# Performance work log

Hardware: AMD Instinct MI355X
Metric: run time of the kernel (lower is better)

The kernel has to match this reference:

```python
import jax, jax.numpy as jnp
import numpy as np

N_NODES = 100000
N_EDGES = 6400000
D_FEAT = 128
HIDDEN = 16


def _gcn_conv(x, row, col, W, b, n):
    # PyG GCNConv: add self-loops, symmetric norm, message from row -> aggregated at col
    h = x @ W  # [N, out]
    loop = jnp.arange(n, dtype=row.dtype)
    r = jnp.concatenate([row, loop])
    c = jnp.concatenate([col, loop])
    ones = jnp.ones(r.shape[0], dtype=x.dtype)
    deg = jax.ops.segment_sum(ones, c, num_segments=n)  # in-degree incl. self-loop
    dinv = jnp.where(deg > 0, jax.lax.rsqrt(deg), 0.0)
    norm = dinv[r] * dinv[c]  # [E+N]
    msg = h[r] * norm[:, None]  # [E+N, out]
    out = jax.ops.segment_sum(msg, c, num_segments=n)
    return out + b


def setup_inputs() -> dict:
    key = jax.random.key(0)
    ks = jax.random.split(key, 8)
    x = jax.random.normal(ks[0], (N_NODES, D_FEAT), dtype=jnp.float32)
    edge_attr = jax.random.normal(ks[1], (N_EDGES, 1), dtype=jnp.float32)
    edge_row = jnp.sort(jax.random.randint(ks[2], (N_EDGES,), 0, N_NODES, dtype=jnp.int32)).astype(jnp.int64)
    edge_col = jax.random.randint(ks[3], (N_EDGES,), 0, N_NODES, dtype=jnp.int32).astype(jnp.int64)
    W1 = jax.random.normal(ks[4], (D_FEAT + 1, HIDDEN), dtype=jnp.float32) * (1.0 / np.sqrt(D_FEAT + 1))
    b1 = jnp.zeros((HIDDEN,), dtype=jnp.float32)
    W2 = jax.random.normal(ks[5], (HIDDEN, 1), dtype=jnp.float32) * (1.0 / np.sqrt(HIDDEN))
    b2 = jnp.zeros((1,), dtype=jnp.float32)
    return {"x": x, "edge_attr": edge_attr, "edge_row": edge_row, "edge_col": edge_col,
            "W1": W1, "b1": b1, "W2": W2, "b2": b2}


def reference(x, edge_attr, edge_row, edge_col, W1, b1, W2, b2):
    n = x.shape[0]
    # the original Python loop == segment-sum of edge_attr by source node (rows are sorted)
    x_edge = jax.ops.segment_sum(edge_attr, edge_row, num_segments=n)  # [N, 1]
    h = jnp.concatenate([x, x_edge], axis=1)  # [N, D+1]
    h = _gcn_conv(h, edge_row, edge_col, W1, b1, n)
    h = jax.nn.relu(h)
    # dropout is identity in eval mode
    out = _gcn_conv(h, edge_row, edge_col, W2, b2, n)  # [N, 1]
    return out
```

## Files before the change

### kernel.cpp

```cpp
#include <hip/hip_runtime.h>


#define D_FEAT 128
#define HIDDEN 16
#define TILE 8192
#define CAP 17408u

__device__ inline float bf2f(unsigned short u) {
    union { unsigned x; float f; } t; t.x = ((unsigned)u) << 16; return t.f;
}

__global__ __launch_bounds__(256) void k_init(float* xe, unsigned* gcur, int n, int nb) {
    int t = blockIdx.x * 256 + threadIdx.x;
    if (t < n) xe[t] = 0.f;
    if (t < nb) gcur[t * 16] = (unsigned)t * CAP;
}

__global__ __launch_bounds__(1024) void k_sortplace(const int* __restrict__ row,
                                                    const int* __restrict__ col,
                                                    const float* __restrict__ ea,
                                                    float* __restrict__ xe,
                                                    unsigned* __restrict__ gcur,
                                                    unsigned* __restrict__ ebufP,
                                                    int ne, int nb) {
    __shared__ unsigned stage[TILE];
    __shared__ unsigned short sbuck[TILE];
    __shared__ unsigned h[512], base_[512], cursor[512], gb_[512];
    __shared__ unsigned wsum[8];
    int tid = threadIdx.x;
    int lane = tid & 63;
    int w = tid >> 6;
    int tile0 = blockIdx.x * TILE;
    int cnt_t = min(TILE, ne - tile0);
    if (tid < 512) h[tid] = 0u;
    __syncthreads();
    int rr[8], cc[8];
    float aa[8];
    #pragma unroll
    for (int k = 0; k < 8; ++k) {
        int e = tile0 + tid + k * 1024;
        if (e < ne) {
            rr[k] = row[e]; cc[k] = col[e]; aa[k] = ea[e];
            atomicAdd(&h[cc[k] >> 8], 1u);
        } else { rr[k] = -1; cc[k] = 0; aa[k] = 0.f; }
    }
    #pragma unroll
    for (int k = 0; k < 8; ++k) {
        int r = rr[k];
        float a = aa[k];
        #pragma unroll
        for (int d = 1; d < 64; d <<= 1) {
            float up = __shfl_up(a, d);
            int  rup = __shfl_up(r, d);
            if (lane >= d && rup == r) a += up;
        }
        int rdn = __shfl_down(r, 1);
        bool tail = (lane == 63) || (rdn != r);
        if (r >= 0 && tail) unsafeAtomicAdd(&xe[r], a);
    }
    __syncthreads();
    unsigned hv = 0, s = 0;
    if (tid < 512) {
        hv = h[tid];
        s = hv;
        #pragma unroll
        for (int d = 1; d < 64; d <<= 1) {
            unsigned u = __shfl_up(s, d);
            if (lane >= d) s += u;
        }
        if (lane == 63) wsum[w] = s;
    }
    __syncthreads();
    if (tid < 512) {
        unsigned woff = 0;
        #pragma unroll
        for (int i = 0; i < 8; ++i) woff += (i < w) ? wsum[i] : 0u;
        unsigned ex = s + woff - hv;
        base_[tid] = ex;
        cursor[tid] = ex;
        if (tid < nb && hv) gb_[tid] = atomicAdd(&gcur[tid * 16], hv);
    }
    __syncthreads();
    #pragma unroll
    for (int k = 0; k < 8; ++k) {
        if (rr[k] >= 0) {
            int b = cc[k] >> 8;
            unsigned p = atomicAdd(&cursor[b], 1u);
            stage[p] = (((unsigned)(cc[k] & 255)) << 24) | (unsigned)rr[k];
            sbuck[p] = (unsigned short)b;
        }
    }
    __syncthreads();
    for (int t = tid; t < cnt_t; t += 1024) {
        unsigned b = sbuck[t];
        unsigned pos = gb_[b] + ((unsigned)t - base_[b]);
        if (pos < (b + 1u) * CAP) ebufP[pos] = stage[t];
    }
}

__global__ __launch_bounds__(1024) void k_deghist(const unsigned* __restrict__ gcur,
                                                  const unsigned* __restrict__ ebufP,
                                                  unsigned* __restrict__ deg,
                                                  unsigned* __restrict__ stG, int n) {
    __shared__ unsigned dg[256];
    __shared__ unsigned wsum[4];
    int tid = threadIdx.x, b = blockIdx.x, lane = tid & 63;
    if (tid < 256) dg[tid] = 0u;
    __syncthreads();
    unsigned base = (unsigned)b * CAP;
    unsigned m = min(gcur[b * 16] - base, CAP);
    unsigned i = tid;
    for (; i + 3072 < m; i += 4096) {
        unsigned pk0 = ebufP[base + i];
        unsigned pk1 = ebufP[base + i + 1024];
        unsigned pk2 = ebufP[base + i + 2048];
        unsigned pk3 = ebufP[base + i + 3072];
        atomicAdd(&dg[pk0 >> 24], 1u);
        atomicAdd(&dg[pk1 >> 24], 1u);
        atomicAdd(&dg[pk2 >> 24], 1u);
        atomicAdd(&dg[pk3 >> 24], 1u);
    }
    for (; i < m; i += 1024) atomicAdd(&dg[ebufP[base + i] >> 24], 1u);
    __syncthreads();
    unsigned dval = 0, s = 0;
    if (tid < 256) {
        dval = dg[tid];
        s = dval;
        #pragma unroll
        for (int d = 1; d < 64; d <<= 1) {
            unsigned uu = __shfl_up(s, d);
            if (lane >= d) s += uu;
        }
        if (lane == 63) wsum[tid >> 6] = s;
    }
    __syncthreads();
    if (tid < 256) {
        int w = tid >> 6;
        unsigned woff = 0;
        #pragma unroll
        for (int i2 = 0; i2 < 4; ++i2) woff += (i2 < w) ? wsum[i2] : 0u;
        unsigned ex = s + woff - dval;
        int v = b * 256 + tid;
        if (v < n) { deg[v] = dval; stG[v] = base + ex; }
    }
}

__global__ __launch_bounds__(256) void k_gemm1(const float* __restrict__ x,
                                               const float* __restrict__ xe,
                                               const unsigned* __restrict__ deg,
                                               const float* __restrict__ W1,
                                               float* __restrict__ g,
                                               unsigned short* __restrict__ gb, int n) {
    __shared__ float WsT[16 * 132];
    __shared__ float xs[64 * 132];
    int tid = threadIdx.x;
    for (int idx = tid; idx < 129 * 16; idx += 256) {
        int k = idx >> 4, j = idx & 15;
        WsT[j * 132 + k] = W1[idx];
    }
    int n0 = blockIdx.x * 64;
    const float4* x4 = (const float4*)x;
    for (int idx = tid; idx < 64 * 32; idx += 256) {
        int r = idx >> 5, c = idx & 31;
        float4 v = (n0 + r < n) ? x4[(size_t)(n0 + r) * 32 + c]
                                : make_float4(0.f, 0.f, 0.f, 0.f);
        *(float4*)&xs[r * 132 + c * 4] = v;
    }
    if (tid < 64) {
        int r = tid;
        xs[r * 132 + 128] = (n0 + r < n) ? xe[n0 + r] : 0.f;
    }
    __syncthreads();
    int j  = tid & 15;
    int nb = tid >> 4;
    const float* wrow = &WsT[j * 132];
    for (int rep = 0; rep < 4; ++rep) {
        int nl = nb + (rep << 4);
        int node = n0 + nl;
        const float* xrow = &xs[nl * 132];
        float acc = 0.f;
        #pragma unroll
        for (int k = 0; k < 128; k += 4) {
            float4 xv = *(const float4*)&xrow[k];
            float4 wv = *(const float4*)&wrow[k];
            acc += xv.x * wv.x;
            acc += xv.y * wv.y;
            acc += xv.z * wv.z;
            acc += xv.w * wv.w;
        }
        acc += xrow[128] * wrow[128];
        if (node < n) {
            float v = acc * rsqrtf((float)deg[node] + 1.0f);
            g[(size_t)node * 16 + j] = v;
            union { float f; unsigned u; } cv; cv.f = v;
            unsigned r16 = (cv.u + 0x7FFFu + ((cv.u >> 16) & 1u)) >> 16;
            gb[(size_t)node * 16 + j] = (unsigned short)r16;
        }
    }
}

__global__ __launch_bounds__(1024) void k_agg1s(const unsigned* __restrict__ gcur,
                                                const unsigned* __restrict__ ebufP,
                                                const unsigned* __restrict__ deg,
                                                const unsigned* __restrict__ stG,
                                                const unsigned* __restrict__ gu,
                                                const float* __restrict__ g,
                                                const float* __restrict__ b1,
                                                const float* __restrict__ W2,
                                                float* __restrict__ g2, int n) {
    __shared__ unsigned sorted[CAP];
    __shared__ unsigned dg[256], st[256], cur[256];
    int tid = threadIdx.x, b = blockIdx.x;
    unsigned base = (unsigned)b * CAP;
    unsigned m = min(gcur[b * 16] - base, CAP);
    if (tid < 256) {
        int v = b * 256 + tid;
        unsigned dval = (v < n) ? deg[v] : 0u;
        unsigned sv   = (v < n) ? stG[v] - base : 0u;
        dg[tid] = dval;
        st[tid] = sv;
        cur[tid] = sv;
    }
    __syncthreads();
    unsigned i = tid;
    for (; i + 3072 < m; i += 4096) {
        unsigned pk0 = ebufP[base + i];
        unsigned pk1 = ebufP[base + i + 1024];
        unsigned pk2 = ebufP[base + i + 2048];
        unsigned pk3 = ebufP[base + i + 3072];
        unsigned p0 = atomicAdd(&cur[pk0 >> 24], 1u);
        unsigned p1 = atomicAdd(&cur[pk1 >> 24], 1u);
        unsigned p2 = atomicAdd(&cur[pk2 >> 24], 1u);
        unsigned p3 = atomicAdd(&cur[pk3 >> 24], 1u);
        if (p0 < CAP) sorted[p0] = pk0 & 0xFFFFFFu;
        if (p1 < CAP) sorted[p1] = pk1 & 0xFFFFFFu;
        if (p2 < CAP) sorted[p2] = pk2 & 0xFFFFFFu;
        if (p3 < CAP) sorted[p3] = pk3 & 0xFFFFFFu;
    }
    for (; i < m; i += 1024) {
        unsigned pk = ebufP[base + i];
        unsigned p = atomicAdd(&cur[pk >> 24], 1u);
        if (p < CAP) sorted[p] = pk & 0xFFFFFFu;
    }
    __syncthreads();
    const uint4* gu4 = (const uint4*)gu;
    int grp = tid >> 4;
    int u = tid & 1;
    int oct = (tid >> 1) & 7;
    float4 bbA = ((const float4*)b1)[2 * u];
    float4 bbB = ((const float4*)b1)[2 * u + 1];
    float4 wwA = ((const float4*)W2)[2 * u];
    float4 wwB = ((const float4*)W2)[2 * u + 1];
    for (int it = 0; it < 4; ++it) {
        int c = it * 64 + grp;
        int v = b * 256 + c;
        if (v >= n) break;
        unsigned s0 = st[c], e0 = s0 + dg[c];
        float a0 = 0.f, a1 = 0.f, a2 = 0.f, a3 = 0.f;
        float a4 = 0.f, a5 = 0.f, a6 = 0.f, a7 = 0.f;
        float c0 = 0.f, c1 = 0.f, c2 = 0.f, c3 = 0.f;
        float c4 = 0.f, c5 = 0.f, c6 = 0.f, c7 = 0.f;
        unsigned q = s0 + oct;
        for (; q + 8 < e0; q += 16) {
            uint4 w0 = gu4[(size_t)sorted[q] * 2 + u];
            uint4 w1 = gu4[(size_t)sorted[q + 8] * 2 + u];
            a0 += bf2f((unsigned short)w0.x); a1 += bf2f((unsigned short)(w0.x >> 16));
            a2 += bf2f((unsigned short)w0.y); a3 += bf2f((unsigned short)(w0.y >> 16));
            a4 += bf2f((unsigned short)w0.z); a5 += bf2f((unsigned short)(w0.z >> 16));
            a6 += bf2f((unsigned short)w0.w); a7 += bf2f((unsigned short)(w0.w >> 16));
            c0 += bf2f((unsigned short)w1.x); c1 += bf2f((unsigned short)(w1.x >> 16));
            c2 += bf2f((unsigned short)w1.y); c3 += bf2f((unsigned short)(w1.y >> 16));
            c4 += bf2f((unsigned short)w1.z); c5 += bf2f((unsigned short)(w1.z >> 16));
            c6 += bf2f((unsigned short)w1.w); c7 += bf2f((unsigned short)(w1.w >> 16));
        }
        for (; q < e0; q += 8) {
            uint4 w0 = gu4[(size_t)sorted[q] * 2 + u];
            a0 += bf2f((unsigned short)w0.x); a1 += bf2f((unsigned short)(w0.x >> 16));
            a2 += bf2f((unsigned short)w0.y); a3 += bf2f((unsigned short)(w0.y >> 16));
            a4 += bf2f((unsigned short)w0.z); a5 += bf2f((unsigned short)(w0.z >> 16));
            a6 += bf2f((unsigned short)w0.w); a7 += bf2f((unsigned short)(w0.w >> 16));
        }
        a0 += c0; a1 += c1; a2 += c2; a3 += c3;
        a4 += c4; a5 += c5; a6 += c6; a7 += c7;
        #pragma unroll
        for (int d = 2; d <= 8; d <<= 1) {
            a0 += __shfl_xor(a0, d, 16);
            a1 += __shfl_xor(a1, d, 16);
            a2 += __shfl_xor(a2, d, 16);
            a3 += __shfl_xor(a3, d, 16);
            a4 += __shfl_xor(a4, d, 16);
            a5 += __shfl_xor(a5, d, 16);
            a6 += __shfl_xor(a6, d, 16);
            a7 += __shfl_xor(a7, d, 16);
        }
        float di = rsqrtf((float)dg[c] + 1.0f);
        float4 gA = ((const float4*)g)[(size_t)v * 4 + 2 * u];
        float4 gB = ((const float4*)g)[(size_t)v * 4 + 2 * u + 1];
        float v0 = fmaxf(di * (gA.x + a0) + bbA.x, 0.f);
        float v1 = fmaxf(di * (gA.y + a1) + bbA.y, 0.f);
        float v2 = fmaxf(di * (gA.z + a2) + bbA.z, 0.f);
        float v3 = fmaxf(di * (gA.w + a3) + bbA.w, 0.f);
        float v4 = fmaxf(di * (gB.x + a4) + bbB.x, 0.f);
        float v5 = fmaxf(di * (gB.y + a5) + bbB.y, 0.f);
        float v6 = fmaxf(di * (gB.z + a6) + bbB.z, 0.f);
        float v7 = fmaxf(di * (gB.w + a7) + bbB.w, 0.f);
        float prd = v0 * wwA.x + v1 * wwA.y + v2 * wwA.z + v3 * wwA.w
                  + v4 * wwB.x + v5 * wwB.y + v6 * wwB.z + v7 * wwB.w;
        prd += __shfl_xor(prd, 1, 16);
        if ((tid & 15) == 0) g2[v] = prd * di;
    }
}

__global__ __launch_bounds__(1024) void k_agg2s(const unsigned* __restrict__ gcur,
                                                const unsigned* __restrict__ ebufP,
                                                const unsigned* __restrict__ deg,
                                                const unsigned* __restrict__ stG,
                                                const float* __restrict__ g2,
                                                const float* __restrict__ b2,
                                                float* __restrict__ out, int n) {
    __shared__ unsigned sorted[CAP];
    __shared__ unsigned dg[256], st[256], cur[256];
    int tid = threadIdx.x, b = blockIdx.x;
    unsigned base = (unsigned)b * CAP;
    unsigned m = min(gcur[b * 16] - base, CAP);
    if (tid < 256) {
        int v = b * 256 + tid;
        unsigned dval = (v < n) ? deg[v] : 0u;
        unsigned sv   = (v < n) ? stG[v] - base : 0u;
        dg[tid] = dval;
        st[tid] = sv;
        cur[tid] = sv;
    }
    __syncthreads();
    unsigned i = tid;
    for (; i + 3072 < m; i += 4096) {
        unsigned pk0 = ebufP[base + i];
        unsigned pk1 = ebufP[base + i + 1024];
        unsigned pk2 = ebufP[base + i + 2048];
        unsigned pk3 = ebufP[base + i + 3072];
        unsigned p0 = atomicAdd(&cur[pk0 >> 24], 1u);
        unsigned p1 = atomicAdd(&cur[pk1 >> 24], 1u);
        unsigned p2 = atomicAdd(&cur[pk2 >> 24], 1u);
        unsigned p3 = atomicAdd(&cur[pk3 >> 24], 1u);
        if (p0 < CAP) sorted[p0] = pk0 & 0xFFFFFFu;
        if (p1 < CAP) sorted[p1] = pk1 & 0xFFFFFFu;
        if (p2 < CAP) sorted[p2] = pk2 & 0xFFFFFFu;
        if (p3 < CAP) sorted[p3] = pk3 & 0xFFFFFFu;
    }
    for (; i < m; i += 1024) {
        unsigned pk = ebufP[base + i];
        unsigned p = atomicAdd(&cur[pk >> 24], 1u);
        if (p < CAP) sorted[p] = pk & 0xFFFFFFu;
    }
    __syncthreads();
    int c = tid >> 2, u = tid & 3;
    int v = b * 256 + c;
    float a0 = 0.f, a1 = 0.f;
    unsigned s0 = st[c], e0 = s0 + dg[c];
    unsigned q = s0 + u;
    for (; q + 4 < e0; q += 8) {
        a0 += g2[sorted[q]];
        a1 += g2[sorted[q + 4]];
    }
    for (; q < e0; q += 4) a0 += g2[sorted[q]];
    float a = a0 + a1;
    a += __shfl_xor(a, 1, 4);
    a += __shfl_xor(a, 2, 4);
    if (u == 0 && v < n) {
        float di = rsqrtf((float)dg[c] + 1.0f);
        out[v] = di * (g2[v] + a) + b2[0];
    }
}

extern "C" void kernel_launch(void* const* d_in, const int* in_sizes, int n_in,
                              void* d_out, int out_size, void* d_ws, size_t ws_size,
                              hipStream_t stream) {
    const float* x   = (const float*)d_in[0];
    const float* ea  = (const float*)d_in[1];
    const int*   row = (const int*)d_in[2];
    const int*   col = (const int*)d_in[3];
    const float* W1  = (const float*)d_in[4];
    const float* b1  = (const float*)d_in[5];
    const float* W2  = (const float*)d_in[6];
    const float* b2  = (const float*)d_in[7];
    float* out = (float*)d_out;

    int n  = in_sizes[0] / D_FEAT;
    int ne = in_sizes[2];
    int nb = (n + 255) >> 8;

    float* ws   = (float*)d_ws;
    float* xe   = ws;
    float* g    = ws + (size_t)n;
    float* g2   = ws + (size_t)17 * n;
    unsigned short* gbuf = (unsigned short*)(ws + (size_t)18 * n);
    unsigned* deg  = (unsigned*)(ws + (size_t)26 * n);
    unsigned* stG  = deg + (size_t)n;
    unsigned* gcur = stG + (size_t)n;
    unsigned* ebufP = gcur + (size_t)nb * 16;

    dim3 blk(256);
    int g_node = (n + 255) / 256;
    int g_tile = (ne + TILE - 1) / TILE;
    int g_gemm = (n + 63) / 64;

    k_init<<<g_node, blk, 0, stream>>>(xe, gcur, n, nb);
    k_sortplace<<<g_tile, 1024, 0, stream>>>(row, col, ea, xe, gcur, ebufP, ne, nb);
    k_deghist<<<nb, 1024, 0, stream>>>(gcur, ebufP, deg, stG, n);
    k_gemm1<<<g_gemm, blk, 0, stream>>>(x, xe, deg, W1, g, gbuf, n);
    k_agg1s<<<nb, 1024, 0, stream>>>(gcur, ebufP, deg, stG, (const unsigned*)gbuf, g, b1, W2, g2, n);
    k_agg2s<<<nb, 1024, 0, stream>>>(gcur, ebufP, deg, stG, g2, b2, out, n);
}
```

Measured before the change: 289.5 us.

## Sort edges per node once and reuse sorted buffer in both aggregations

```diff
diff --git a/kernel.cpp b/kernel.cpp
--- a/kernel.cpp
+++ b/kernel.cpp
@@ -98,29 +98,30 @@
     }
 }
 
-__global__ __launch_bounds__(1024) void k_deghist(const unsigned* __restrict__ gcur,
-                                                  const unsigned* __restrict__ ebufP,
-                                                  unsigned* __restrict__ deg,
-                                                  unsigned* __restrict__ stG, int n) {
-    __shared__ unsigned dg[256];
+__global__ __launch_bounds__(1024) void k_sortnode(const unsigned* __restrict__ gcur,
+                                                   const unsigned* __restrict__ ebufP,
+                                                   unsigned* __restrict__ deg,
+                                                   unsigned* __restrict__ stG,
+                                                   unsigned* __restrict__ sortedG, int n) {
+    __shared__ unsigned sorted[CAP];
+    __shared__ unsigned dg[256], cur[256];
     __shared__ unsigned wsum[4];
     int tid = threadIdx.x, b = blockIdx.x, lane = tid & 63;
     if (tid < 256) dg[tid] = 0u;
     __syncthreads();
     unsigned base = (unsigned)b * CAP;
     unsigned m = min(gcur[b * 16] - base, CAP);
-    unsigned i = tid;
-    for (; i + 3072 < m; i += 4096) {
-        unsigned pk0 = ebufP[base + i];
-        unsigned pk1 = ebufP[base + i + 1024];
-        unsigned pk2 = ebufP[base + i + 2048];
-        unsigned pk3 = ebufP[base + i + 3072];
-        atomicAdd(&dg[pk0 >> 24], 1u);
-        atomicAdd(&dg[pk1 >> 24], 1u);
-        atomicAdd(&dg[pk2 >> 24], 1u);
-        atomicAdd(&dg[pk3 >> 24], 1u);
-    }
-    for (; i < m; i += 1024) atomicAdd(&dg[ebufP[base + i] >> 24], 1u);
+    unsigned mt = m & ~3u;
+    const uint4* eb4 = (const uint4*)(ebufP + base);
+    for (unsigned t = tid; t * 4 + 3 < m; t += 1024) {
+        uint4 pk = eb4[t];
+        atomicAdd(&dg[pk.x >> 24], 1u);
+        atomicAdd(&dg[pk.y >> 24], 1u);
+        atomicAdd(&dg[pk.z >> 24], 1u);
+        atomicAdd(&dg[pk.w >> 24], 1u);
+    }
+    for (unsigned t = mt + tid; t < m; t += 1024)
+        atomicAdd(&dg[ebufP[base + t] >> 24], 1u);
     __syncthreads();
     unsigned dval = 0, s = 0;
     if (tid < 256) {
@@ -142,7 +143,31 @@
         unsigned ex = s + woff - dval;
         int v = b * 256 + tid;
         if (v < n) { deg[v] = dval; stG[v] = base + ex; }
-    }
+        cur[tid] = ex;
+    }
+    __syncthreads();
+    for (unsigned t = tid; t * 4 + 3 < m; t += 1024) {
+        uint4 pk = eb4[t];
+        unsigned p0 = atomicAdd(&cur[pk.x >> 24], 1u);
+        unsigned p1 = atomicAdd(&cur[pk.y >> 24], 1u);
+        unsigned p2 = atomicAdd(&cur[pk.z >> 24], 1u);
+        unsigned p3 = atomicAdd(&cur[pk.w >> 24], 1u);
+        sorted[p0] = pk.x & 0xFFFFFFu;
+        sorted[p1] = pk.y & 0xFFFFFFu;
+        sorted[p2] = pk.z & 0xFFFFFFu;
+        sorted[p3] = pk.w & 0xFFFFFFu;
+    }
+    for (unsigned t = mt + tid; t < m; t += 1024) {
+        unsigned pk = ebufP[base + t];
+        unsigned p = atomicAdd(&cur[pk >> 24], 1u);
+        sorted[p] = pk & 0xFFFFFFu;
+    }
+    __syncthreads();
+    uint4* sg4 = (uint4*)(sortedG + base);
+    for (unsigned t = tid; t * 4 + 3 < m; t += 1024)
+        sg4[t] = *(const uint4*)&sorted[t * 4];
+    for (unsigned t = mt + tid; t < m; t += 1024)
+        sortedG[base + t] = sorted[t];
 }
 
 __global__ __launch_bounds__(256) void k_gemm1(const float* __restrict__ x,
@@ -200,7 +225,7 @@
 }
 
 __global__ __launch_bounds__(1024) void k_agg1s(const unsigned* __restrict__ gcur,
-                                                const unsigned* __restrict__ ebufP,
+                                                const unsigned* __restrict__ sortedG,
                                                 const unsigned* __restrict__ deg,
                                                 const unsigned* __restrict__ stG,
                                                 const unsigned* __restrict__ gu,
@@ -209,39 +234,21 @@
                                                 const float* __restrict__ W2,
                                                 float* __restrict__ g2, int n) {
     __shared__ unsigned sorted[CAP];
-    __shared__ unsigned dg[256], st[256], cur[256];
+    __shared__ unsigned dg[256], st[256];
     int tid = threadIdx.x, b = blockIdx.x;
     unsigned base = (unsigned)b * CAP;
     unsigned m = min(gcur[b * 16] - base, CAP);
     if (tid < 256) {
         int v = b * 256 + tid;
-        unsigned dval = (v < n) ? deg[v] : 0u;
-        unsigned sv   = (v < n) ? stG[v] - base : 0u;
-        dg[tid] = dval;
-        st[tid] = sv;
-        cur[tid] = sv;
-    }
-    __syncthreads();
-    unsigned i = tid;
-    for (; i + 3072 < m; i += 4096) {
-        unsigned pk0 = ebufP[base + i];
-        unsigned pk1 = ebufP[base + i + 1024];
-        unsigned pk2 = ebufP[base + i + 2048];
-        unsigned pk3 = ebufP[base + i + 3072];
-        unsigned p0 = atomicAdd(&cur[pk0 >> 24], 1u);
-        unsigned p1 = atomicAdd(&cur[pk1 >> 24], 1u);
-        unsigned p2 = atomicAdd(&cur[pk2 >> 24], 1u);
-        unsigned p3 = atomicAdd(&cur[pk3 >> 24], 1u);
-        if (p0 < CAP) sorted[p0] = pk0 & 0xFFFFFFu;
-        if (p1 < CAP) sorted[p1] = pk1 & 0xFFFFFFu;
-        if (p2 < CAP) sorted[p2] = pk2 & 0xFFFFFFu;
-        if (p3 < CAP) sorted[p3] = pk3 & 0xFFFFFFu;
-    }
-    for (; i < m; i += 1024) {
-        unsigned pk = ebufP[base + i];
-        unsigned p = atomicAdd(&cur[pk >> 24], 1u);
-        if (p < CAP) sorted[p] = pk & 0xFFFFFFu;
-    }
+        dg[tid] = (v < n) ? deg[v] : 0u;
+        st[tid] = (v < n) ? stG[v] - base : 0u;
+    }
+    unsigned mt = m & ~3u;
+    const uint4* sg4 = (const uint4*)(sortedG + base);
+    for (unsigned t = tid; t * 4 + 3 < m; t += 1024)
+        *(uint4*)&sorted[t * 4] = sg4[t];
+    for (unsigned t = mt + tid; t < m; t += 1024)
+        sorted[t] = sortedG[base + t];
     __syncthreads();
     const uint4* gu4 = (const uint4*)gu;
     int grp = tid >> 4;
@@ -312,46 +319,28 @@
 }
 
 __global__ __launch_bounds__(1024) void k_agg2s(const unsigned* __restrict__ gcur,
-                                                const unsigned* __restrict__ ebufP,
+                                                const unsigned* __restrict__ sortedG,
                                                 const unsigned* __restrict__ deg,
                                                 const unsigned* __restrict__ stG,
                                                 const float* __restrict__ g2,
                                                 const float* __restrict__ b2,
                                                 float* __restrict__ out, int n) {
     __shared__ unsigned sorted[CAP];
-    __shared__ unsigned dg[256], st[256], cur[256];
+    __shared__ unsigned dg[256], st[256];
     int tid = threadIdx.x, b = blockIdx.x;
     unsigned base = (unsigned)b * CAP;
     unsigned m = min(gcur[b * 16] - base, CAP);
     if (tid < 256) {
         int v = b * 256 + tid;
-        unsigned dval = (v < n) ? deg[v] : 0u;
-        unsigned sv   = (v < n) ? stG[v] - base : 0u;
-        dg[tid] = dval;
-        st[tid] = sv;
-        cur[tid] = sv;
-    }
-    __syncthreads();
-    unsigned i = tid;
-    for (; i + 3072 < m; i += 4096) {
-        unsigned pk0 = ebufP[base + i];
-        unsigned pk1 = ebufP[base + i + 1024];
-        unsigned pk2 = ebufP[base + i + 2048];
-        unsigned pk3 = ebufP[base + i + 3072];
-        unsigned p0 = atomicAdd(&cur[pk0 >> 24], 1u);
-        unsigned p1 = atomicAdd(&cur[pk1 >> 24], 1u);
-        unsigned p2 = atomicAdd(&cur[pk2 >> 24], 1u);
-        unsigned p3 = atomicAdd(&cur[pk3 >> 24], 1u);
-        if (p0 < CAP) sorted[p0] = pk0 & 0xFFFFFFu;
-        if (p1 < CAP) sorted[p1] = pk1 & 0xFFFFFFu;
-        if (p2 < CAP) sorted[p2] = pk2 & 0xFFFFFFu;
-        if (p3 < CAP) sorted[p3] = pk3 & 0xFFFFFFu;
-    }
-    for (; i < m; i += 1024) {
-        unsigned pk = ebufP[base + i];
-        unsigned p = atomicAdd(&cur[pk >> 24], 1u);
-        if (p < CAP) sorted[p] = pk & 0xFFFFFFu;
-    }
+        dg[tid] = (v < n) ? deg[v] : 0u;
+        st[tid] = (v < n) ? stG[v] - base : 0u;
+    }
+    unsigned mt = m & ~3u;
+    const uint4* sg4 = (const uint4*)(sortedG + base);
+    for (unsigned t = tid; t * 4 + 3 < m; t += 1024)
+        *(uint4*)&sorted[t * 4] = sg4[t];
+    for (unsigned t = mt + tid; t < m; t += 1024)
+        sorted[t] = sortedG[base + t];
     __syncthreads();
     int c = tid >> 2, u = tid & 3;
     int v = b * 256 + c;
@@ -397,7 +386,8 @@
     unsigned* deg  = (unsigned*)(ws + (size_t)26 * n);
     unsigned* stG  = deg + (size_t)n;
     unsigned* gcur = stG + (size_t)n;
-    unsigned* ebufP = gcur + (size_t)nb * 16;
+    unsigned* ebufP   = gcur + (size_t)nb * 16;
+    unsigned* sortedG = ebufP + (size_t)nb * CAP;
 
     dim3 blk(256);
     int g_node = (n + 255) / 256;
@@ -406,8 +396,8 @@
 
     k_init<<<g_node, blk, 0, stream>>>(xe, gcur, n, nb);
     k_sortplace<<<g_tile, 1024, 0, stream>>>(row, col, ea, xe, gcur, ebufP, ne, nb);
-    k_deghist<<<nb, 1024, 0, stream>>>(gcur, ebufP, deg, stG, n);
+    k_sortnode<<<nb, 1024, 0, stream>>>(gcur, ebufP, deg, stG, sortedG, n);
     k_gemm1<<<g_gemm, blk, 0, stream>>>(x, xe, deg, W1, g, gbuf, n);
-    k_agg1s<<<nb, 1024, 0, stream>>>(gcur, ebufP, deg, stG, (const unsigned*)gbuf, g, b1, W2, g2, n);
-    k_agg2s<<<nb, 1024, 0, stream>>>(gcur, ebufP, deg, stG, g2, b2, out, n);
-}
+    k_agg1s<<<nb, 1024, 0, stream>>>(gcur, sortedG, deg, stG, (const unsigned*)gbuf, g, b1, W2, g2, n);
+    k_agg2s<<<nb, 1024, 0, stream>>>(gcur, sortedG, deg, stG, g2, b2, out, n);
+}
```

After: 294.9 us. About the same (+1.8%).
